# Kernel optimization log

Hardware: AMD Instinct MI355X
Metric: run time of the kernel (lower is better)

The kernel has to match this reference:

```python
import jax, jax.numpy as jnp
import numpy as np

N = 20000      # nodes
E = 320000     # directed edges (avg degree 16)
H = 4          # GAT attention heads
IN, HID, OUT = 5, 64, 32
DIMS = [(HID, HID), (HID, HID), (HID, OUT)]  # per-layer (in, out_per_head)


def setup_inputs() -> dict:
    keys = iter(jax.random.split(jax.random.key(0), 64))

    def rn(shape, s=0.1):
        return jax.random.normal(next(keys), shape, jnp.float32) * s

    inp = {
        "x": jax.random.normal(next(keys), (N, IN), jnp.float32),
        "edge_index": jax.random.randint(next(keys), (2, E), 0, N, dtype=jnp.int32),
        "enc_W": rn((IN, HID)), "enc_b": rn((HID,)),
    }
    for l, (din, dout) in enumerate(DIMS):
        inp["W%d" % l] = rn((din, H * dout))
        inp["as%d" % l] = rn((H, dout))
        inp["ad%d" % l] = rn((H, dout))
        inp["b%d" % l] = rn((dout,))
        inp["g%d" % l] = 1.0 + rn((dout,))
        inp["be%d" % l] = rn((dout,))
        inp["m%d" % l] = rn((dout,))
        inp["v%d" % l] = 1.0 + 0.1 * jax.random.uniform(next(keys), (dout,), jnp.float32)
    for h in ("eth", "man"):
        inp[h + "_W1"] = rn((OUT, OUT // 2)); inp[h + "_b1"] = rn((OUT // 2,))
        inp[h + "_W2"] = rn((OUT // 2, 1)); inp[h + "_b2"] = rn((1,))
    return inp


def _gat(x, src, dst, W, a_s, a_d, bias, n):
    # PyG GATConv: heads=H, concat=False (head mean), leaky_relu slope 0.2
    xp = (x @ W).reshape(n, H, -1)                        # [N,H,C]
    al_s = (xp * a_s).sum(-1)                             # [N,H]
    al_d = (xp * a_d).sum(-1)                             # [N,H]
    e = jax.nn.leaky_relu(al_s[src] + al_d[dst], 0.2)     # [E',H]
    emax = jax.ops.segment_max(e, dst, num_segments=n)    # stable softmax over in-edges
    ee = jnp.exp(e - emax[dst])
    den = jax.ops.segment_sum(ee, dst, num_segments=n)
    alpha = ee / (den[dst] + 1e-16)                       # [E',H]
    out = jax.ops.segment_sum(alpha[:, :, None] * xp[src], dst, num_segments=n)
    return out.mean(axis=1) + bias                        # [N,C]


def _bn(x, g, b, m, v):
    # BatchNorm1d, eval mode with running stats
    return (x - m) / jnp.sqrt(v + 1e-5) * g + b


def _head(z, W1, b1, W2, b2):
    # Linear -> ReLU -> (dropout off) -> Linear -> Sigmoid
    return jax.nn.sigmoid(jax.nn.relu(z @ W1 + b1) @ W2 + b2)


def _forward(x, src, dst, enc_W, enc_b, Ws, ASs, ADs, Bs, Gs, BEs, Ms, Vs, eth, man):
    n = x.shape[0]
    h = x @ enc_W + enc_b
    for l in range(3):
        h = _gat(h, src, dst, Ws[l], ASs[l], ADs[l], Bs[l], n)
        h = _bn(h, Gs[l], BEs[l], Ms[l], Vs[l])
        if l < 2:
            h = jax.nn.relu(h)
    graph_emb = h.mean(axis=0, keepdims=True)             # no `batch` attr branch
    ethics = _head(graph_emb, *eth)
    manip = _head(graph_emb, *man)
    return h, graph_emb, ethics, manip


def reference(x, edge_index, enc_W, enc_b,
              W0, as0, ad0, b0, g0, be0, m0, v0,
              W1, as1, ad1, b1, g1, be1, m1, v1,
              W2, as2, ad2, b2, g2, be2, m2, v2,
              eth_W1, eth_b1, eth_W2, eth_b2,
              man_W1, man_b1, man_W2, man_b2):
    n = x.shape[0]
    loops = jnp.arange(n, dtype=edge_index.dtype)
    src = jnp.concatenate([edge_index[0], loops])         # GATConv adds self-loops
    dst = jnp.concatenate([edge_index[1], loops])
    return _forward(x, src, dst, enc_W, enc_b,
                    [W0, W1, W2], [as0, as1, as2], [ad0, ad1, ad2], [b0, b1, b2],
                    [g0, g1, g2], [be0, be1, be2], [m0, m1, m2], [v0, v1, v2],
                    (eth_W1, eth_b1, eth_W2, eth_b2),
                    (man_W1, man_b1, man_W2, man_b2))
```

## Files before the change

### kernel.cpp

```cpp
#include <hip/hip_runtime.h>
#include <math.h>


#define H4 4

static __device__ __forceinline__ unsigned short f2bf(float f) {
  unsigned u = __float_as_uint(f);
  u += 0x7fffu + ((u >> 16) & 1u);
  return (unsigned short)(u >> 16);
}

static __device__ __forceinline__ float bfh(unsigned u) {
  return __uint_as_float(u << 16);
}
static __device__ __forceinline__ float bfl(unsigned u) {
  return __uint_as_float(u & 0xffff0000u);
}

__global__ void k_count(const int* __restrict__ dst, int* __restrict__ deg, int E) {
  int gid = blockIdx.x * blockDim.x + threadIdx.x;
  if (gid < E) atomicAdd(&deg[dst[gid]], 1);
}

__global__ void k_alloc(int* __restrict__ cursor, int* __restrict__ rbeg,
                        int* __restrict__ rend, int* __restrict__ col,
                        int* __restrict__ counter, int N,
                        const float* __restrict__ W0, const float* __restrict__ as0, const float* __restrict__ ad0,
                        const float* __restrict__ W1, const float* __restrict__ as1, const float* __restrict__ ad1,
                        const float* __restrict__ W2, const float* __restrict__ as2, const float* __restrict__ ad2,
                        float* __restrict__ pas, float* __restrict__ pad) {
  int gid = blockIdx.x * blockDim.x + threadIdx.x;
  int lane = threadIdx.x & 63;
  int size = (gid < N) ? (cursor[gid] + 1) : 0;
  int v = size;
#pragma unroll
  for (int off = 1; off < 64; off <<= 1) {
    int t = __shfl_up(v, off, 64);
    if (lane >= off) v += t;
  }
  int tot = __shfl(v, 63, 64);
  int base = 0;
  if (lane == 63) base = atomicAdd(counter, tot);
  base = __shfl(base, 63, 64);
  if (gid < N) {
    int p = base + v - size;
    rbeg[gid] = p;
    rend[gid] = p + size;
    col[p] = gid;
    cursor[gid] = p + 1;
  }
  if (blockIdx.x < 3) {
    int l = blockIdx.x;
    const float* W  = (l == 0) ? W0 : (l == 1) ? W1 : W2;
    const float* ap = (l == 0) ? as0 : (l == 1) ? as1 : as2;
    const float* dp = (l == 0) ? ad0 : (l == 1) ? ad1 : ad2;
    int HC = (l == 2) ? 128 : 256;
    int C  = HC / H4;
    int tid = threadIdx.x;
    int k = tid >> 2, h = tid & 3;
    float vs = 0.f, vd = 0.f;
    for (int c = 0; c < C; ++c) {
      float w = W[k * HC + h * C + c];
      vs += w * ap[h * C + c];
      vd += w * dp[h * C + c];
    }
    pas[l * 256 + tid] = vs;
    pad[l * 256 + tid] = vd;
  }
}

__global__ void k_scatter(const int* __restrict__ src, const int* __restrict__ dst,
                          int* __restrict__ cursor, int* __restrict__ col, int E) {
  int gid = blockIdx.x * blockDim.x + threadIdx.x;
  if (gid < E) {
    int p = atomicAdd(&cursor[dst[gid]], 1);
    col[p] = src[gid];
  }
}

template <int HC, bool ENC>
__global__ void k_gemm_al(const float* __restrict__ hin,
                          const float* __restrict__ encW, const float* __restrict__ encb,
                          const float* __restrict__ W,
                          const float* __restrict__ was, const float* __restrict__ wad,
                          unsigned short* __restrict__ xpb,
                          float* __restrict__ als, float* __restrict__ ald, int N) {
  constexpr int K = 64, NB = 16;
  __shared__ float hs[NB * K];
  int n0 = blockIdx.x * NB;
  int tid = threadIdx.x;
  if (ENC) {
    for (int idx = tid; idx < NB * K; idx += HC) {
      int i = idx >> 6, j = idx & 63;
      int n = n0 + i;
      float a = 0.f;
      if (n < N) {
        a = encb[j];
#pragma unroll
        for (int k = 0; k < 5; ++k) a += hin[n * 5 + k] * encW[k * 64 + j];
      }
      hs[idx] = a;
    }
  } else {
    for (int idx = tid; idx < NB * K; idx += HC) {
      int n = n0 + (idx >> 6);
      hs[idx] = (n < N) ? hin[(size_t)n0 * K + idx] : 0.f;
    }
  }
  __syncthreads();
  float acc[NB];
#pragma unroll
  for (int i = 0; i < NB; ++i) acc[i] = 0.f;
  for (int k = 0; k < K; k += 4) {
    float w0 = W[(k + 0) * HC + tid];
    float w1 = W[(k + 1) * HC + tid];
    float w2 = W[(k + 2) * HC + tid];
    float w3 = W[(k + 3) * HC + tid];
#pragma unroll
    for (int i = 0; i < NB; ++i) {
      float4 hv = *(const float4*)&hs[i * K + k];
      acc[i] += hv.x * w0 + hv.y * w1 + hv.z * w2 + hv.w * w3;
    }
  }
#pragma unroll
  for (int i = 0; i < NB; ++i) {
    int n = n0 + i;
    if (n < N) xpb[(size_t)n * HC + tid] = f2bf(acc[i]);
  }
  if (tid < NB * H4) {
    int i = tid >> 2, h = tid & 3;
    int n = n0 + i;
    float vs = 0.f, vd = 0.f;
#pragma unroll 8
    for (int k = 0; k < K; ++k) {
      float hv = hs[i * K + k];
      vs += hv * was[k * 4 + h];
      vd += hv * wad[k * 4 + h];
    }
    if (n < N) {
      als[n * H4 + h] = vs;
      ald[n * H4 + h] = vd;
    }
  }
}

template <int C, bool RELU, bool POOL>
__global__ __launch_bounds__(128) void k_gather(
    const unsigned short* __restrict__ xpb,
    const float* __restrict__ als, const float* __restrict__ ald,
    const int* __restrict__ rbeg, const int* __restrict__ rend,
    const int* __restrict__ col,
    const float* __restrict__ bias, const float* __restrict__ g,
    const float* __restrict__ be, const float* __restrict__ m,
    const float* __restrict__ v, float* __restrict__ hout,
    float* __restrict__ gpart, int N) {
  constexpr int HC = H4 * C;
  constexpr int VPL = HC / 64;
  __shared__ float accbuf[HC];
  __shared__ float sbuf[H4];
  int sub = threadIdx.x >> 6;
  int lane = threadIdx.x & 63;
  int n = blockIdx.x;
  int h = lane >> 4;
  float aldn = ald[n * H4 + h];
  int beg = rbeg[n], end = rend[n];
  int len = end - beg;
  int lenA = (len + 1) >> 1;
  int jb = sub ? (beg + lenA) : beg;
  int je = sub ? end : (beg + lenA);

  float s = 0.f;
  float acc[VPL];
#pragma unroll
  for (int i = 0; i < VPL; ++i) acc[i] = 0.f;

  int j = jb;
  for (; j + 3 < je; j += 4) {
    int s0 = col[j], s1 = col[j + 1], s2 = col[j + 2], s3 = col[j + 3];
    float a0 = als[s0 * H4 + h], a1 = als[s1 * H4 + h];
    float a2 = als[s2 * H4 + h], a3 = als[s3 * H4 + h];
    float e0 = a0 + aldn; e0 = (e0 > 0.f) ? e0 : 0.2f * e0; e0 = __expf(e0);
    float e1 = a1 + aldn; e1 = (e1 > 0.f) ? e1 : 0.2f * e1; e1 = __expf(e1);
    float e2 = a2 + aldn; e2 = (e2 > 0.f) ? e2 : 0.2f * e2; e2 = __expf(e2);
    float e3 = a3 + aldn; e3 = (e3 > 0.f) ? e3 : 0.2f * e3; e3 = __expf(e3);
    s += (e0 + e1) + (e2 + e3);
    if constexpr (VPL == 4) {
      uint2 u0 = *(const uint2*)(xpb + (size_t)s0 * HC + lane * 4);
      uint2 u1 = *(const uint2*)(xpb + (size_t)s1 * HC + lane * 4);
      uint2 u2 = *(const uint2*)(xpb + (size_t)s2 * HC + lane * 4);
      uint2 u3 = *(const uint2*)(xpb + (size_t)s3 * HC + lane * 4);
      acc[0] += e0 * bfh(u0.x) + e1 * bfh(u1.x) + e2 * bfh(u2.x) + e3 * bfh(u3.x);
      acc[1] += e0 * bfl(u0.x) + e1 * bfl(u1.x) + e2 * bfl(u2.x) + e3 * bfl(u3.x);
      acc[2] += e0 * bfh(u0.y) + e1 * bfh(u1.y) + e2 * bfh(u2.y) + e3 * bfh(u3.y);
      acc[3] += e0 * bfl(u0.y) + e1 * bfl(u1.y) + e2 * bfl(u2.y) + e3 * bfl(u3.y);
    } else {
      unsigned u0 = *(const unsigned*)(xpb + (size_t)s0 * HC + lane * 2);
      unsigned u1 = *(const unsigned*)(xpb + (size_t)s1 * HC + lane * 2);
      unsigned u2 = *(const unsigned*)(xpb + (size_t)s2 * HC + lane * 2);
      unsigned u3 = *(const unsigned*)(xpb + (size_t)s3 * HC + lane * 2);
      acc[0] += e0 * bfh(u0) + e1 * bfh(u1) + e2 * bfh(u2) + e3 * bfh(u3);
      acc[1] += e0 * bfl(u0) + e1 * bfl(u1) + e2 * bfl(u2) + e3 * bfl(u3);
    }
  }
  for (; j < je; ++j) {
    int s0 = col[j];
    float a0 = als[s0 * H4 + h];
    float e0 = a0 + aldn; e0 = (e0 > 0.f) ? e0 : 0.2f * e0; e0 = __expf(e0);
    s += e0;
    if constexpr (VPL == 4) {
      uint2 u0 = *(const uint2*)(xpb + (size_t)s0 * HC + lane * 4);
      acc[0] += e0 * bfh(u0.x);
      acc[1] += e0 * bfl(u0.x);
      acc[2] += e0 * bfh(u0.y);
      acc[3] += e0 * bfl(u0.y);
    } else {
      unsigned u0 = *(const unsigned*)(xpb + (size_t)s0 * HC + lane * 2);
      acc[0] += e0 * bfh(u0);
      acc[1] += e0 * bfl(u0);
    }
  }

  if (sub) {
    if ((lane & 15) == 0) sbuf[h] = s;
#pragma unroll
    for (int i = 0; i < VPL; ++i) accbuf[lane * VPL + i] = acc[i];
  }
  __syncthreads();
  if (sub) return;
  s += sbuf[h];
#pragma unroll
  for (int i = 0; i < VPL; ++i) acc[i] += accbuf[lane * VPL + i];

  float inv = 1.f / (s + 1e-16f);
#pragma unroll
  for (int i = 0; i < VPL; ++i) {
    acc[i] *= inv;
    acc[i] += __shfl_xor(acc[i], 16, 64);
    acc[i] += __shfl_xor(acc[i], 32, 64);
  }

  if (lane < 16) {
    int c0 = lane * VPL;
    float o[VPL];
#pragma unroll
    for (int i = 0; i < VPL; ++i) {
      int cc = c0 + i;
      float t = acc[i] * (1.f / H4) + bias[cc];
      t = (t - m[cc]) * rsqrtf(v[cc] + 1e-5f) * g[cc] + be[cc];
      if (RELU) t = fmaxf(t, 0.f);
      o[i] = t;
      if (POOL) atomicAdd(&gpart[(blockIdx.x & 255) * 32 + cc], t);
    }
    if constexpr (VPL == 4)
      *(float4*)&hout[(size_t)n * C + c0] = make_float4(o[0], o[1], o[2], o[3]);
    else
      *(float2*)&hout[(size_t)n * C + c0] = make_float2(o[0], o[1]);
  }
}

__global__ void k_heads2(const float* __restrict__ gpart,
                         const float* __restrict__ eW1, const float* __restrict__ eb1,
                         const float* __restrict__ eW2, const float* __restrict__ eb2,
                         const float* __restrict__ mW1, const float* __restrict__ mb1,
                         const float* __restrict__ mW2, const float* __restrict__ mb2,
                         float* __restrict__ out, int N) {
  __shared__ float red[256];
  __shared__ float z[32];
  __shared__ float hid[32];
  int tid = threadIdx.x;
  int c = tid & 31;
  float s = 0.f;
  for (int b = tid >> 5; b < 256; b += 8) s += gpart[b * 32 + c];
  red[tid] = s;
  __syncthreads();
  size_t base = (size_t)N * 32;
  if (tid < 32) {
    float t = 0.f;
#pragma unroll
    for (int i = 0; i < 8; ++i) t += red[i * 32 + tid];
    t /= (float)N;
    z[tid] = t;
    out[base + tid] = t;
  }
  __syncthreads();
  if (tid < 16) {
    float a = eb1[tid], b = mb1[tid];
    for (int k = 0; k < 32; ++k) {
      a += z[k] * eW1[k * 16 + tid];
      b += z[k] * mW1[k * 16 + tid];
    }
    hid[tid] = fmaxf(a, 0.f);
    hid[16 + tid] = fmaxf(b, 0.f);
  }
  __syncthreads();
  if (tid == 0) {
    float a = eb2[0];
    for (int k = 0; k < 16; ++k) a += hid[k] * eW2[k];
    out[base + 32] = 1.f / (1.f + __expf(-a));
  } else if (tid == 1) {
    float a = mb2[0];
    for (int k = 0; k < 16; ++k) a += hid[16 + k] * mW2[k];
    out[base + 33] = 1.f / (1.f + __expf(-a));
  }
}

extern "C" void kernel_launch(void* const* d_in, const int* in_sizes, int n_in,
                              void* d_out, int out_size, void* d_ws, size_t ws_size,
                              hipStream_t stream) {
  const int N = in_sizes[0] / 5;
  const int E = in_sizes[1] / 2;
  const int M = E + N;

  const float* x = (const float*)d_in[0];
  const int* ei = (const int*)d_in[1];
  const int* e_src = ei;
  const int* e_dst = ei + E;
  const float* encW = (const float*)d_in[2];
  const float* encb = (const float*)d_in[3];
  const float* Wl[3]; const float* asl[3]; const float* adl[3]; const float* bl[3];
  const float* gl[3]; const float* bel[3]; const float* ml[3]; const float* vl[3];
  for (int l = 0; l < 3; ++l) {
    const int o = 4 + 8 * l;
    Wl[l]  = (const float*)d_in[o + 0];
    asl[l] = (const float*)d_in[o + 1];
    adl[l] = (const float*)d_in[o + 2];
    bl[l]  = (const float*)d_in[o + 3];
    gl[l]  = (const float*)d_in[o + 4];
    bel[l] = (const float*)d_in[o + 5];
    ml[l]  = (const float*)d_in[o + 6];
    vl[l]  = (const float*)d_in[o + 7];
  }
  const float* eW1 = (const float*)d_in[28];
  const float* eb1 = (const float*)d_in[29];
  const float* eW2 = (const float*)d_in[30];
  const float* eb2 = (const float*)d_in[31];
  const float* mW1 = (const float*)d_in[32];
  const float* mb1 = (const float*)d_in[33];
  const float* mW2 = (const float*)d_in[34];
  const float* mb2 = (const float*)d_in[35];

  float* out = (float*)d_out;

  float* wf = (float*)d_ws;
  size_t off = 0;
  float* hA   = wf + off; off += (size_t)N * 64;
  float* hB   = wf + off; off += (size_t)N * 64;
  unsigned short* xpb = (unsigned short*)(wf + off); off += (size_t)N * 128;
  float* als  = wf + off; off += (size_t)N * 4;
  float* ald  = wf + off; off += (size_t)N * 4;
  float* pas  = wf + off; off += 3 * 256;
  float* pad  = wf + off; off += 3 * 256;
  int* wi = (int*)(wf + off);
  int* col     = wi;
  int* rbeg    = col + M;
  int* rend    = rbeg + N;
  int* cursor  = rend + N;
  int* counter = cursor + N;
  float* gpart = (float*)(counter + 1);

  const int T = 256;
  const int gE  = (E + T - 1) / T;
  const int gN  = (N + T - 1) / T;
  const int gGE = (N + 15) / 16;

  hipMemsetAsync(cursor, 0, (size_t)(N + 1) * sizeof(int) + 256 * 32 * sizeof(float), stream);
  k_count<<<gE, T, 0, stream>>>(e_dst, cursor, E);
  k_alloc<<<gN, T, 0, stream>>>(cursor, rbeg, rend, col, counter, N,
                                Wl[0], asl[0], adl[0], Wl[1], asl[1], adl[1],
                                Wl[2], asl[2], adl[2], pas, pad);
  k_scatter<<<gE, T, 0, stream>>>(e_src, e_dst, cursor, col, E);

  k_gemm_al<256, true><<<gGE, 256, 0, stream>>>(x, encW, encb, Wl[0], pas, pad,
                                                xpb, als, ald, N);
  k_gather<64, true, false><<<N, 128, 0, stream>>>(xpb, als, ald, rbeg, rend, col,
                                                   bl[0], gl[0], bel[0], ml[0], vl[0],
                                                   hB, gpart, N);

  k_gemm_al<256, false><<<gGE, 256, 0, stream>>>(hB, encW, encb, Wl[1], pas + 256, pad + 256,
                                                 xpb, als, ald, N);
  k_gather<64, true, false><<<N, 128, 0, stream>>>(xpb, als, ald, rbeg, rend, col,
                                                   bl[1], gl[1], bel[1], ml[1], vl[1],
                                                   hA, gpart, N);

  k_gemm_al<128, false><<<gGE, 128, 0, stream>>>(hA, encW, encb, Wl[2], pas + 512, pad + 512,
                                                 xpb, als, ald, N);
  k_gather<32, false, true><<<N, 128, 0, stream>>>(xpb, als, ald, rbeg, rend, col,
                                                   bl[2], gl[2], bel[2], ml[2], vl[2],
                                                   out, gpart, N);

  k_heads2<<<1, 256, 0, stream>>>(gpart, eW1, eb1, eW2, eb2, mW1, mb1, mW2, mb2, out, N);
}
```

Before: 332.9 us.

## Fuse whole GAT forward into one persistent cooperative kernel with grid syncs

Replaces the sequence of separate kernel launches (memset, CSR build, three gemm/gather pairs, heads) with a single cooperative persistent kernel that separates stages with grid.sync. The degree count runs concurrently with the first-layer GEMM on disjoint block subsets, and the gather switches from a two-wavefront-per-node block to one wavefront per node with a grid-stride loop. This removes launch overhead and inter-kernel gaps, but adds grid barrier costs and limits the grid to resident blocks, which may reduce latency hiding in the memory-bound gathers. A fallback multi-kernel path is kept in case the cooperative launch fails.

```diff
diff --git a/kernel.cpp b/kernel.cpp
--- a/kernel.cpp
+++ b/kernel.cpp
@@ -1,20 +1,316 @@
 #include <hip/hip_runtime.h>
+#include <hip/hip_cooperative_groups.h>
 #include <math.h>
 
 
+namespace cg = cooperative_groups;
+
 #define H4 4
+constexpr int TB = 256;
 
 static __device__ __forceinline__ unsigned short f2bf(float f) {
   unsigned u = __float_as_uint(f);
   u += 0x7fffu + ((u >> 16) & 1u);
   return (unsigned short)(u >> 16);
 }
-
-static __device__ __forceinline__ float bfh(unsigned u) {
-  return __uint_as_float(u << 16);
-}
-static __device__ __forceinline__ float bfl(unsigned u) {
-  return __uint_as_float(u & 0xffff0000u);
+static __device__ __forceinline__ float bfh(unsigned u) { return __uint_as_float(u << 16); }
+static __device__ __forceinline__ float bfl(unsigned u) { return __uint_as_float(u & 0xffff0000u); }
+
+struct Pr {
+  const float* x; const int* esrc; const int* edst;
+  const float* encW; const float* encb;
+  const float* W[3]; const float* as_[3]; const float* ad[3];
+  const float* b[3]; const float* g[3]; const float* be[3];
+  const float* m[3]; const float* v[3];
+  const float* eW1; const float* eb1; const float* eW2; const float* eb2;
+  const float* mW1; const float* mb1; const float* mW2; const float* mb2;
+  float* hA; float* hB; unsigned short* xpb; float* als; float* ald;
+  float* pas; float* pad; float* gpart;
+  int* col; int* rbeg; int* rend; int* cursor; int* counter;
+  float* out; int N; int E;
+};
+
+
+template <int HC, bool ENC>
+__device__ void gemm_stage(const Pr& p, const float* hin, const float* W,
+                           const float* was, const float* wad, float* hs,
+                           int bstart, int bnum) {
+  int b = (int)blockIdx.x - bstart;
+  if (b < 0 || b >= bnum) return;
+  int tid = threadIdx.x;
+  int ntile = (p.N + 15) >> 4;
+  for (int t = b; t < ntile; t += bnum) {
+    int n0 = t << 4;
+    for (int idx = tid; idx < 1024; idx += TB) {
+      int i = idx >> 6, j = idx & 63;
+      int n = n0 + i;
+      float a = 0.f;
+      if (ENC) {
+        if (n < p.N) {
+          a = p.encb[j];
+#pragma unroll
+          for (int k = 0; k < 5; ++k) a += p.x[n * 5 + k] * p.encW[k * 64 + j];
+        }
+      } else {
+        a = (n < p.N) ? hin[(size_t)n * 64 + j] : 0.f;
+      }
+      hs[idx] = a;
+    }
+    __syncthreads();
+    if (tid < HC) {
+      float acc[16];
+#pragma unroll
+      for (int i = 0; i < 16; ++i) acc[i] = 0.f;
+      for (int k = 0; k < 64; k += 4) {
+        float w0 = W[(k + 0) * HC + tid];
+        float w1 = W[(k + 1) * HC + tid];
+        float w2 = W[(k + 2) * HC + tid];
+        float w3 = W[(k + 3) * HC + tid];
+#pragma unroll
+        for (int i = 0; i < 16; ++i) {
+          float4 hv = *(const float4*)&hs[i * 64 + k];
+          acc[i] += hv.x * w0 + hv.y * w1 + hv.z * w2 + hv.w * w3;
+        }
+      }
+#pragma unroll
+      for (int i = 0; i < 16; ++i) {
+        int n = n0 + i;
+        if (n < p.N) p.xpb[(size_t)n * HC + tid] = f2bf(acc[i]);
+      }
+    }
+    if (tid < 64) {
+      int i = tid >> 2, h = tid & 3;
+      int n = n0 + i;
+      float vs = 0.f, vd = 0.f;
+#pragma unroll 8
+      for (int k = 0; k < 64; ++k) {
+        float hv = hs[i * 64 + k];
+        vs += hv * was[k * 4 + h];
+        vd += hv * wad[k * 4 + h];
+      }
+      if (n < p.N) {
+        p.als[n * H4 + h] = vs;
+        p.ald[n * H4 + h] = vd;
+      }
+    }
+    __syncthreads();
+  }
+}
+
+template <int C, bool RELU, bool POOL>
+__device__ void gather_stage(const Pr& p, float* hout, const float* bias,
+                             const float* g, const float* be, const float* m,
+                             const float* v) {
+  constexpr int HC = H4 * C;
+  constexpr int VPL = HC / 64;
+  int lane = threadIdx.x & 63;
+  int h = lane >> 4;
+  int wid = blockIdx.x * 4 + (threadIdx.x >> 6);
+  int wstride = gridDim.x * 4;
+  for (int n = wid; n < p.N; n += wstride) {
+    float aldn = p.ald[n * H4 + h];
+    int beg = p.rbeg[n], end = p.rend[n];
+    float s = 0.f;
+    float acc[VPL];
+#pragma unroll
+    for (int i = 0; i < VPL; ++i) acc[i] = 0.f;
+    int j = beg;
+    for (; j + 3 < end; j += 4) {
+      int s0 = p.col[j], s1 = p.col[j + 1], s2 = p.col[j + 2], s3 = p.col[j + 3];
+      float a0 = p.als[s0 * H4 + h], a1 = p.als[s1 * H4 + h];
+      float a2 = p.als[s2 * H4 + h], a3 = p.als[s3 * H4 + h];
+      float e0 = a0 + aldn; e0 = (e0 > 0.f) ? e0 : 0.2f * e0; e0 = __expf(e0);
+      float e1 = a1 + aldn; e1 = (e1 > 0.f) ? e1 : 0.2f * e1; e1 = __expf(e1);
+      float e2 = a2 + aldn; e2 = (e2 > 0.f) ? e2 : 0.2f * e2; e2 = __expf(e2);
+      float e3 = a3 + aldn; e3 = (e3 > 0.f) ? e3 : 0.2f * e3; e3 = __expf(e3);
+      s += (e0 + e1) + (e2 + e3);
+      if constexpr (VPL == 4) {
+        uint2 u0 = *(const uint2*)(p.xpb + (size_t)s0 * HC + lane * 4);
+        uint2 u1 = *(const uint2*)(p.xpb + (size_t)s1 * HC + lane * 4);
+        uint2 u2 = *(const uint2*)(p.xpb + (size_t)s2 * HC + lane * 4);
+        uint2 u3 = *(const uint2*)(p.xpb + (size_t)s3 * HC + lane * 4);
+        acc[0] += e0 * bfh(u0.x) + e1 * bfh(u1.x) + e2 * bfh(u2.x) + e3 * bfh(u3.x);
+        acc[1] += e0 * bfl(u0.x) + e1 * bfl(u1.x) + e2 * bfl(u2.x) + e3 * bfl(u3.x);
+        acc[2] += e0 * bfh(u0.y) + e1 * bfh(u1.y) + e2 * bfh(u2.y) + e3 * bfh(u3.y);
+        acc[3] += e0 * bfl(u0.y) + e1 * bfl(u1.y) + e2 * bfl(u2.y) + e3 * bfl(u3.y);
+      } else {
+        unsigned u0 = *(const unsigned*)(p.xpb + (size_t)s0 * HC + lane * 2);
+        unsigned u1 = *(const unsigned*)(p.xpb + (size_t)s1 * HC + lane * 2);
+        unsigned u2 = *(const unsigned*)(p.xpb + (size_t)s2 * HC + lane * 2);
+        unsigned u3 = *(const unsigned*)(p.xpb + (size_t)s3 * HC + lane * 2);
+        acc[0] += e0 * bfh(u0) + e1 * bfh(u1) + e2 * bfh(u2) + e3 * bfh(u3);
+        acc[1] += e0 * bfl(u0) + e1 * bfl(u1) + e2 * bfl(u2) + e3 * bfl(u3);
+      }
+    }
+    for (; j < end; ++j) {
+      int s0 = p.col[j];
+      float a0 = p.als[s0 * H4 + h];
+      float e0 = a0 + aldn; e0 = (e0 > 0.f) ? e0 : 0.2f * e0; e0 = __expf(e0);
+      s += e0;
+      if constexpr (VPL == 4) {
+        uint2 u0 = *(const uint2*)(p.xpb + (size_t)s0 * HC + lane * 4);
+        acc[0] += e0 * bfh(u0.x);
+        acc[1] += e0 * bfl(u0.x);
+        acc[2] += e0 * bfh(u0.y);
+        acc[3] += e0 * bfl(u0.y);
+      } else {
+        unsigned u0 = *(const unsigned*)(p.xpb + (size_t)s0 * HC + lane * 2);
+        acc[0] += e0 * bfh(u0);
+        acc[1] += e0 * bfl(u0);
+      }
+    }
+    float inv = 1.f / (s + 1e-16f);
+#pragma unroll
+    for (int i = 0; i < VPL; ++i) {
+      acc[i] *= inv;
+      acc[i] += __shfl_xor(acc[i], 16, 64);
+      acc[i] += __shfl_xor(acc[i], 32, 64);
+    }
+    if (lane < 16) {
+      int c0 = lane * VPL;
+      float o[VPL];
+#pragma unroll
+      for (int i = 0; i < VPL; ++i) {
+        int cc = c0 + i;
+        float t = acc[i] * (1.f / H4) + bias[cc];
+        t = (t - m[cc]) * rsqrtf(v[cc] + 1e-5f) * g[cc] + be[cc];
+        if (RELU) t = fmaxf(t, 0.f);
+        o[i] = t;
+        if (POOL) atomicAdd(&p.gpart[(n & 255) * 32 + cc], t);
+      }
+      if constexpr (VPL == 4)
+        *(float4*)&hout[(size_t)n * C + c0] = make_float4(o[0], o[1], o[2], o[3]);
+      else
+        *(float2*)&hout[(size_t)n * C + c0] = make_float2(o[0], o[1]);
+    }
+  }
+}
+
+__global__ __launch_bounds__(TB, 4) void mega(Pr p) {
+  cg::grid_group grid = cg::this_grid();
+  __shared__ float hs[1024];
+  const int tid = threadIdx.x;
+  const int lane = tid & 63;
+  const int GBx = gridDim.x;
+  const int gtid = blockIdx.x * TB + tid;
+  const int GS = GBx * TB;
+
+  {
+    int Z = p.N + 1 + 256 * 32;
+    int* zb = p.cursor;
+    for (int i = gtid; i < Z; i += GS) zb[i] = 0;
+    if (blockIdx.x < 3) {
+      int l = blockIdx.x;
+      const float* W = p.W[l];
+      const float* ap = p.as_[l];
+      const float* dp = p.ad[l];
+      int HC = (l == 2) ? 128 : 256;
+      int C = HC / H4;
+      int k = tid >> 2, h = tid & 3;
+      float vs = 0.f, vd = 0.f;
+      for (int c = 0; c < C; ++c) {
+        float w = W[k * HC + h * C + c];
+        vs += w * ap[h * C + c];
+        vd += w * dp[h * C + c];
+      }
+      p.pas[l * 256 + tid] = vs;
+      p.pad[l * 256 + tid] = vd;
+    }
+  }
+  grid.sync();
+
+  {
+    int cnt = GBx >> 2;
+    if ((int)blockIdx.x < cnt) {
+      for (int i = blockIdx.x * TB + tid; i < p.E; i += cnt * TB)
+        atomicAdd(&p.cursor[p.edst[i]], 1);
+    } else {
+      gemm_stage<256, true>(p, p.x, p.W[0], p.pas, p.pad, hs, cnt, GBx - cnt);
+    }
+  }
+  grid.sync();
+
+  for (int base = blockIdx.x * TB + (tid & ~63); base < p.N; base += GS) {
+    int gid = base + lane;
+    int dval = (gid < p.N) ? atomicAdd(&p.cursor[gid], 0) : -1;
+    int size = (gid < p.N) ? dval + 1 : 0;
+    int v = size;
+#pragma unroll
+    for (int off = 1; off < 64; off <<= 1) {
+      int t = __shfl_up(v, off, 64);
+      if (lane >= off) v += t;
+    }
+    int tot = __shfl(v, 63, 64);
+    int b0 = 0;
+    if (lane == 63) b0 = atomicAdd(p.counter, tot);
+    b0 = __shfl(b0, 63, 64);
+    if (gid < p.N) {
+      int pos = b0 + v - size;
+      p.rbeg[gid] = pos;
+      p.rend[gid] = pos + size;
+      p.col[pos] = gid;
+      p.cursor[gid] = pos + 1;
+    }
+  }
+  grid.sync();
+
+  for (int i = gtid; i < p.E; i += GS) {
+    int pos = atomicAdd(&p.cursor[p.edst[i]], 1);
+    p.col[pos] = p.esrc[i];
+  }
+  grid.sync();
+
+  gather_stage<64, true, false>(p, p.hB, p.b[0], p.g[0], p.be[0], p.m[0], p.v[0]);
+  grid.sync();
+  gemm_stage<256, false>(p, p.hB, p.W[1], p.pas + 256, p.pad + 256, hs, 0, GBx);
+  grid.sync();
+  gather_stage<64, true, false>(p, p.hA, p.b[1], p.g[1], p.be[1], p.m[1], p.v[1]);
+  grid.sync();
+  gemm_stage<128, false>(p, p.hA, p.W[2], p.pas + 512, p.pad + 512, hs, 0, GBx);
+  grid.sync();
+  gather_stage<32, false, true>(p, p.out, p.b[2], p.g[2], p.be[2], p.m[2], p.v[2]);
+  grid.sync();
+
+  if (blockIdx.x == 0) {
+    float* red = hs;
+    float* z = hs + 256;
+    float* hid = hs + 288;
+    int c = tid & 31;
+    float sAcc = 0.f;
+    for (int bkt = tid >> 5; bkt < 256; bkt += 8)
+      sAcc += atomicAdd(&p.gpart[bkt * 32 + c], 0.f);
+    red[tid] = sAcc;
+    __syncthreads();
+    size_t base = (size_t)p.N * 32;
+    if (tid < 32) {
+      float t = 0.f;
+#pragma unroll
+      for (int i = 0; i < 8; ++i) t += red[i * 32 + tid];
+      t /= (float)p.N;
+      z[tid] = t;
+      p.out[base + tid] = t;
+    }
+    __syncthreads();
+    if (tid < 16) {
+      float a = p.eb1[tid], b = p.mb1[tid];
+      for (int k = 0; k < 32; ++k) {
+        a += z[k] * p.eW1[k * 16 + tid];
+        b += z[k] * p.mW1[k * 16 + tid];
+      }
+      hid[tid] = fmaxf(a, 0.f);
+      hid[16 + tid] = fmaxf(b, 0.f);
+    }
+    __syncthreads();
+    if (tid == 0) {
+      float a = p.eb2[0];
+      for (int k = 0; k < 16; ++k) a += hid[k] * p.eW2[k];
+      p.out[base + 32] = 1.f / (1.f + __expf(-a));
+    } else if (tid == 1) {
+      float a = p.mb2[0];
+      for (int k = 0; k < 16; ++k) a += hid[16 + k] * p.mW2[k];
+      p.out[base + 33] = 1.f / (1.f + __expf(-a));
+    }
+  }
 }
 
 __global__ void k_count(const int* __restrict__ dst, int* __restrict__ deg, int E) {
@@ -22,16 +318,10 @@
   if (gid < E) atomicAdd(&deg[dst[gid]], 1);
 }
 
-__global__ void k_alloc(int* __restrict__ cursor, int* __restrict__ rbeg,
-                        int* __restrict__ rend, int* __restrict__ col,
-                        int* __restrict__ counter, int N,
-                        const float* __restrict__ W0, const float* __restrict__ as0, const float* __restrict__ ad0,
-                        const float* __restrict__ W1, const float* __restrict__ as1, const float* __restrict__ ad1,
-                        const float* __restrict__ W2, const float* __restrict__ as2, const float* __restrict__ ad2,
-                        float* __restrict__ pas, float* __restrict__ pad) {
+__global__ void k_alloc(Pr p) {
   int gid = blockIdx.x * blockDim.x + threadIdx.x;
   int lane = threadIdx.x & 63;
-  int size = (gid < N) ? (cursor[gid] + 1) : 0;
+  int size = (gid < p.N) ? (p.cursor[gid] + 1) : 0;
   int v = size;
 #pragma unroll
   for (int off = 1; off < 64; off <<= 1) {
@@ -39,23 +329,23 @@
     if (lane >= off) v += t;
   }
   int tot = __shfl(v, 63, 64);
-  int base = 0;
-  if (lane == 63) base = atomicAdd(counter, tot);
-  base = __shfl(base, 63, 64);
-  if (gid < N) {
-    int p = base + v - size;
-    rbeg[gid] = p;
-    rend[gid] = p + size;
-    col[p] = gid;
-    cursor[gid] = p + 1;
+  int b0 = 0;
+  if (lane == 63) b0 = atomicAdd(p.counter, tot);
+  b0 = __shfl(b0, 63, 64);
+  if (gid < p.N) {
+    int pos = b0 + v - size;
+    p.rbeg[gid] = pos;
+    p.rend[gid] = pos + size;
+    p.col[pos] = gid;
+    p.cursor[gid] = pos + 1;
   }
   if (blockIdx.x < 3) {
     int l = blockIdx.x;
-    const float* W  = (l == 0) ? W0 : (l == 1) ? W1 : W2;
-    const float* ap = (l == 0) ? as0 : (l == 1) ? as1 : as2;
-    const float* dp = (l == 0) ? ad0 : (l == 1) ? ad1 : ad2;
+    const float* W = p.W[l];
+    const float* ap = p.as_[l];
+    const float* dp = p.ad[l];
     int HC = (l == 2) ? 128 : 256;
-    int C  = HC / H4;
+    int C = HC / H4;
     int tid = threadIdx.x;
     int k = tid >> 2, h = tid & 3;
     float vs = 0.f, vd = 0.f;
@@ -64,8 +354,8 @@
       vs += w * ap[h * C + c];
       vd += w * dp[h * C + c];
     }
-    pas[l * 256 + tid] = vs;
-    pad[l * 256 + tid] = vd;
+    p.pas[l * 256 + tid] = vs;
+    p.pad[l * 256 + tid] = vd;
   }
 }
 
@@ -79,228 +369,60 @@
 }
 
 template <int HC, bool ENC>
-__global__ void k_gemm_al(const float* __restrict__ hin,
-                          const float* __restrict__ encW, const float* __restrict__ encb,
-                          const float* __restrict__ W,
-                          const float* __restrict__ was, const float* __restrict__ wad,
-                          unsigned short* __restrict__ xpb,
-                          float* __restrict__ als, float* __restrict__ ald, int N) {
-  constexpr int K = 64, NB = 16;
-  __shared__ float hs[NB * K];
-  int n0 = blockIdx.x * NB;
-  int tid = threadIdx.x;
-  if (ENC) {
-    for (int idx = tid; idx < NB * K; idx += HC) {
-      int i = idx >> 6, j = idx & 63;
-      int n = n0 + i;
-      float a = 0.f;
-      if (n < N) {
-        a = encb[j];
-#pragma unroll
-        for (int k = 0; k < 5; ++k) a += hin[n * 5 + k] * encW[k * 64 + j];
-      }
-      hs[idx] = a;
-    }
-  } else {
-    for (int idx = tid; idx < NB * K; idx += HC) {
-      int n = n0 + (idx >> 6);
-      hs[idx] = (n < N) ? hin[(size_t)n0 * K + idx] : 0.f;
-    }
-  }
-  __syncthreads();
-  float acc[NB];
-#pragma unroll
-  for (int i = 0; i < NB; ++i) acc[i] = 0.f;
-  for (int k = 0; k < K; k += 4) {
-    float w0 = W[(k + 0) * HC + tid];
-    float w1 = W[(k + 1) * HC + tid];
-    float w2 = W[(k + 2) * HC + tid];
-    float w3 = W[(k + 3) * HC + tid];
-#pragma unroll
-    for (int i = 0; i < NB; ++i) {
-      float4 hv = *(const float4*)&hs[i * K + k];
-      acc[i] += hv.x * w0 + hv.y * w1 + hv.z * w2 + hv.w * w3;
-    }
-  }
-#pragma unroll
-  for (int i = 0; i < NB; ++i) {
-    int n = n0 + i;
-    if (n < N) xpb[(size_t)n * HC + tid] = f2bf(acc[i]);
-  }
-  if (tid < NB * H4) {
-    int i = tid >> 2, h = tid & 3;
-    int n = n0 + i;
-    float vs = 0.f, vd = 0.f;
-#pragma unroll 8
-    for (int k = 0; k < K; ++k) {
-      float hv = hs[i * K + k];
-      vs += hv * was[k * 4 + h];
-      vd += hv * wad[k * 4 + h];
-    }
-    if (n < N) {
-      als[n * H4 + h] = vs;
-      ald[n * H4 + h] = vd;
-    }
-  }
+__global__ void k_gemm_al(Pr p, const float* __restrict__ hin, const float* __restrict__ W,
+                          const float* __restrict__ was, const float* __restrict__ wad) {
+  __shared__ float hs[1024];
+  gemm_stage<HC, ENC>(p, hin, W, was, wad, hs, 0, gridDim.x);
 }
 
 template <int C, bool RELU, bool POOL>
-__global__ __launch_bounds__(128) void k_gather(
-    const unsigned short* __restrict__ xpb,
-    const float* __restrict__ als, const float* __restrict__ ald,
-    const int* __restrict__ rbeg, const int* __restrict__ rend,
-    const int* __restrict__ col,
-    const float* __restrict__ bias, const float* __restrict__ g,
-    const float* __restrict__ be, const float* __restrict__ m,
-    const float* __restrict__ v, float* __restrict__ hout,
-    float* __restrict__ gpart, int N) {
-  constexpr int HC = H4 * C;
-  constexpr int VPL = HC / 64;
-  __shared__ float accbuf[HC];
-  __shared__ float sbuf[H4];
-  int sub = threadIdx.x >> 6;
-  int lane = threadIdx.x & 63;
-  int n = blockIdx.x;
-  int h = lane >> 4;
-  float aldn = ald[n * H4 + h];
-  int beg = rbeg[n], end = rend[n];
-  int len = end - beg;
-  int lenA = (len + 1) >> 1;
-  int jb = sub ? (beg + lenA) : beg;
-  int je = sub ? end : (beg + lenA);
-
-  float s = 0.f;
-  float acc[VPL];
-#pragma unroll
-  for (int i = 0; i < VPL; ++i) acc[i] = 0.f;
-
-  int j = jb;
-  for (; j + 3 < je; j += 4) {
-    int s0 = col[j], s1 = col[j + 1], s2 = col[j + 2], s3 = col[j + 3];
-    float a0 = als[s0 * H4 + h], a1 = als[s1 * H4 + h];
-    float a2 = als[s2 * H4 + h], a3 = als[s3 * H4 + h];
-    float e0 = a0 + aldn; e0 = (e0 > 0.f) ? e0 : 0.2f * e0; e0 = __expf(e0);
-    float e1 = a1 + aldn; e1 = (e1 > 0.f) ? e1 : 0.2f * e1; e1 = __expf(e1);
-    float e2 = a2 + aldn; e2 = (e2 > 0.f) ? e2 : 0.2f * e2; e2 = __expf(e2);
-    float e3 = a3 + aldn; e3 = (e3 > 0.f) ? e3 : 0.2f * e3; e3 = __expf(e3);
-    s += (e0 + e1) + (e2 + e3);
-    if constexpr (VPL == 4) {
-      uint2 u0 = *(const uint2*)(xpb + (size_t)s0 * HC + lane * 4);
-      uint2 u1 = *(const uint2*)(xpb + (size_t)s1 * HC + lane * 4);
-      uint2 u2 = *(const uint2*)(xpb + (size_t)s2 * HC + lane * 4);
-      uint2 u3 = *(const uint2*)(xpb + (size_t)s3 * HC + lane * 4);
-      acc[0] += e0 * bfh(u0.x) + e1 * bfh(u1.x) + e2 * bfh(u2.x) + e3 * bfh(u3.x);
-      acc[1] += e0 * bfl(u0.x) + e1 * bfl(u1.x) + e2 * bfl(u2.x) + e3 * bfl(u3.x);
-      acc[2] += e0 * bfh(u0.y) + e1 * bfh(u1.y) + e2 * bfh(u2.y) + e3 * bfh(u3.y);
-      acc[3] += e0 * bfl(u0.y) + e1 * bfl(u1.y) + e2 * bfl(u2.y) + e3 * bfl(u3.y);
-    } else {
-      unsigned u0 = *(const unsigned*)(xpb + (size_t)s0 * HC + lane * 2);
-      unsigned u1 = *(const unsigned*)(xpb + (size_t)s1 * HC + lane * 2);
-      unsigned u2 = *(const unsigned*)(xpb + (size_t)s2 * HC + lane * 2);
-      unsigned u3 = *(const unsigned*)(xpb + (size_t)s3 * HC + lane * 2);
-      acc[0] += e0 * bfh(u0) + e1 * bfh(u1) + e2 * bfh(u2) + e3 * bfh(u3);
-      acc[1] += e0 * bfl(u0) + e1 * bfl(u1) + e2 * bfl(u2) + e3 * bfl(u3);
-    }
-  }
-  for (; j < je; ++j) {
-    int s0 = col[j];
-    float a0 = als[s0 * H4 + h];
-    float e0 = a0 + aldn; e0 = (e0 > 0.f) ? e0 : 0.2f * e0; e0 = __expf(e0);
-    s += e0;
-    if constexpr (VPL == 4) {
-      uint2 u0 = *(const uint2*)(xpb + (size_t)s0 * HC + lane * 4);
-      acc[0] += e0 * bfh(u0.x);
-      acc[1] += e0 * bfl(u0.x);
-      acc[2] += e0 * bfh(u0.y);
-      acc[3] += e0 * bfl(u0.y);
-    } else {
-      unsigned u0 = *(const unsigned*)(xpb + (size_t)s0 * HC + lane * 2);
-      acc[0] += e0 * bfh(u0);
-      acc[1] += e0 * bfl(u0);
-    }
-  }
-
-  if (sub) {
-    if ((lane & 15) == 0) sbuf[h] = s;
-#pragma unroll
-    for (int i = 0; i < VPL; ++i) accbuf[lane * VPL + i] = acc[i];
-  }
-  __syncthreads();
-  if (sub) return;
-  s += sbuf[h];
-#pragma unroll
-  for (int i = 0; i < VPL; ++i) acc[i] += accbuf[lane * VPL + i];
-
-  float inv = 1.f / (s + 1e-16f);
-#pragma unroll
-  for (int i = 0; i < VPL; ++i) {
-    acc[i] *= inv;
-    acc[i] += __shfl_xor(acc[i], 16, 64);
-    acc[i] += __shfl_xor(acc[i], 32, 64);
-  }
-
-  if (lane < 16) {
-    int c0 = lane * VPL;
-    float o[VPL];
-#pragma unroll
-    for (int i = 0; i < VPL; ++i) {
-      int cc = c0 + i;
-      float t = acc[i] * (1.f / H4) + bias[cc];
-      t = (t - m[cc]) * rsqrtf(v[cc] + 1e-5f) * g[cc] + be[cc];
-      if (RELU) t = fmaxf(t, 0.f);
-      o[i] = t;
-      if (POOL) atomicAdd(&gpart[(blockIdx.x & 255) * 32 + cc], t);
-    }
-    if constexpr (VPL == 4)
-      *(float4*)&hout[(size_t)n * C + c0] = make_float4(o[0], o[1], o[2], o[3]);
-    else
-      *(float2*)&hout[(size_t)n * C + c0] = make_float2(o[0], o[1]);
-  }
-}
-
-__global__ void k_heads2(const float* __restrict__ gpart,
-                         const float* __restrict__ eW1, const float* __restrict__ eb1,
-                         const float* __restrict__ eW2, const float* __restrict__ eb2,
-                         const float* __restrict__ mW1, const float* __restrict__ mb1,
-                         const float* __restrict__ mW2, const float* __restrict__ mb2,
-                         float* __restrict__ out, int N) {
+__global__ __launch_bounds__(256) void k_gather(Pr p, float* hout,
+                                                const float* __restrict__ bias,
+                                                const float* __restrict__ g,
+                                                const float* __restrict__ be,
+                                                const float* __restrict__ m,
+                                                const float* __restrict__ v) {
+  gather_stage<C, RELU, POOL>(p, hout, bias, g, be, m, v);
+}
+
+__global__ void k_heads2(Pr p) {
   __shared__ float red[256];
   __shared__ float z[32];
   __shared__ float hid[32];
   int tid = threadIdx.x;
   int c = tid & 31;
   float s = 0.f;
-  for (int b = tid >> 5; b < 256; b += 8) s += gpart[b * 32 + c];
+  for (int b = tid >> 5; b < 256; b += 8) s += p.gpart[b * 32 + c];
   red[tid] = s;
   __syncthreads();
-  size_t base = (size_t)N * 32;
+  size_t base = (size_t)p.N * 32;
   if (tid < 32) {
     float t = 0.f;
 #pragma unroll
     for (int i = 0; i < 8; ++i) t += red[i * 32 + tid];
-    t /= (float)N;
+    t /= (float)p.N;
     z[tid] = t;
-    out[base + tid] = t;
+    p.out[base + tid] = t;
   }
   __syncthreads();
   if (tid < 16) {
-    float a = eb1[tid], b = mb1[tid];
+    float a = p.eb1[tid], b = p.mb1[tid];
     for (int k = 0; k < 32; ++k) {
-      a += z[k] * eW1[k * 16 + tid];
-      b += z[k] * mW1[k * 16 + tid];
+      a += z[k] * p.eW1[k * 16 + tid];
+      b += z[k] * p.mW1[k * 16 + tid];
     }
     hid[tid] = fmaxf(a, 0.f);
     hid[16 + tid] = fmaxf(b, 0.f);
   }
   __syncthreads();
   if (tid == 0) {
-    float a = eb2[0];
-    for (int k = 0; k < 16; ++k) a += hid[k] * eW2[k];
-    out[base + 32] = 1.f / (1.f + __expf(-a));
+    float a = p.eb2[0];
+    for (int k = 0; k < 16; ++k) a += hid[k] * p.eW2[k];
+    p.out[base + 32] = 1.f / (1.f + __expf(-a));
   } else if (tid == 1) {
-    float a = mb2[0];
-    for (int k = 0; k < 16; ++k) a += hid[16 + k] * mW2[k];
-    out[base + 33] = 1.f / (1.f + __expf(-a));
+    float a = p.mb2[0];
+    for (int k = 0; k < 16; ++k) a += hid[16 + k] * p.mW2[k];
+    p.out[base + 33] = 1.f / (1.f + __expf(-a));
   }
 }
 
@@ -311,82 +433,78 @@
   const int E = in_sizes[1] / 2;
   const int M = E + N;
 
-  const float* x = (const float*)d_in[0];
+  Pr p;
+  p.x = (const float*)d_in[0];
   const int* ei = (const int*)d_in[1];
-  const int* e_src = ei;
-  const int* e_dst = ei + E;
-  const float* encW = (const float*)d_in[2];
-  const float* encb = (const float*)d_in[3];
-  const float* Wl[3]; const float* asl[3]; const float* adl[3]; const float* bl[3];
-  const float* gl[3]; const float* bel[3]; const float* ml[3]; const float* vl[3];
+  p.esrc = ei;
+  p.edst = ei + E;
+  p.encW = (const float*)d_in[2];
+  p.encb = (const float*)d_in[3];
   for (int l = 0; l < 3; ++l) {
     const int o = 4 + 8 * l;
-    Wl[l]  = (const float*)d_in[o + 0];
-    asl[l] = (const float*)d_in[o + 1];
-    adl[l] = (const float*)d_in[o + 2];
-    bl[l]  = (const float*)d_in[o + 3];
-    gl[l]  = (const float*)d_in[o + 4];
-    bel[l] = (const float*)d_in[o + 5];
-    ml[l]  = (const float*)d_in[o + 6];
-    vl[l]  = (const float*)d_in[o + 7];
-  }
-  const float* eW1 = (const float*)d_in[28];
-  const float* eb1 = (const float*)d_in[29];
-  const float* eW2 = (const float*)d_in[30];
-  const float* eb2 = (const float*)d_in[31];
-  const float* mW1 = (const float*)d_in[32];
-  const float* mb1 = (const float*)d_in[33];
-  const float* mW2 = (const float*)d_in[34];
-  const float* mb2 = (const float*)d_in[35];
-
-  float* out = (float*)d_out;
+    p.W[l]  = (const float*)d_in[o + 0];
+    p.as_[l] = (const float*)d_in[o + 1];
+    p.ad[l] = (const float*)d_in[o + 2];
+    p.b[l]  = (const float*)d_in[o + 3];
+    p.g[l]  = (const float*)d_in[o + 4];
+    p.be[l] = (const float*)d_in[o + 5];
+    p.m[l]  = (const float*)d_in[o + 6];
+    p.v[l]  = (const float*)d_in[o + 7];
+  }
+  p.eW1 = (const float*)d_in[28]; p.eb1 = (const float*)d_in[29];
+  p.eW2 = (const float*)d_in[30]; p.eb2 = (const float*)d_in[31];
+  p.mW1 = (const float*)d_in[32]; p.mb1 = (const float*)d_in[33];
+  p.mW2 = (const float*)d_in[34]; p.mb2 = (const float*)d_in[35];
+  p.out = (float*)d_out;
+  p.N = N; p.E = E;
 
   float* wf = (float*)d_ws;
   size_t off = 0;
-  float* hA   = wf + off; off += (size_t)N * 64;
-  float* hB   = wf + off; off += (size_t)N * 64;
-  unsigned short* xpb = (unsigned short*)(wf + off); off += (size_t)N * 128;
-  float* als  = wf + off; off += (size_t)N * 4;
-  float* ald  = wf + off; off += (size_t)N * 4;
-  float* pas  = wf + off; off += 3 * 256;
-  float* pad  = wf + off; off += 3 * 256;
+  p.hA = wf + off; off += (size_t)N * 64;
+  p.hB = wf + off; off += (size_t)N * 64;
+  p.xpb = (unsigned short*)(wf + off); off += (size_t)N * 128;
+  p.als = wf + off; off += (size_t)N * 4;
+  p.ald = wf + off; off += (size_t)N * 4;
+  p.pas = wf + off; off += 3 * 256;
+  p.pad = wf + off; off += 3 * 256;
   int* wi = (int*)(wf + off);
-  int* col     = wi;
-  int* rbeg    = col + M;
-  int* rend    = rbeg + N;
-  int* cursor  = rend + N;
-  int* counter = cursor + N;
-  float* gpart = (float*)(counter + 1);
+  p.col = wi;
+  p.rbeg = wi + M;
+  p.rend = p.rbeg + N;
+  p.cursor = p.rend + N;
+  p.counter = p.cursor + N;
+  p.gpart = (float*)(p.counter + 1);
+
+  hipError_t st = hipErrorUnknown;
+  int maxB = 0;
+  if (hipOccupancyMaxActiveBlocksPerMultiprocessor(&maxB, (const void*)mega, TB, 0)
+      != hipSuccess) maxB = 0;
+  if (maxB > 4) maxB = 4;
+  int gb = maxB * 256;
+  if (gb >= 256) {
+    void* args[] = {&p};
+    st = hipLaunchCooperativeKernel((const void*)mega, dim3(gb), dim3(TB), args, 0, stream);
+  }
+  if (st == hipSuccess) return;
 
   const int T = 256;
-  const int gE  = (E + T - 1) / T;
-  const int gN  = (N + T - 1) / T;
+  const int gE = (E + T - 1) / T;
+  const int gN = (N + T - 1) / T;
   const int gGE = (N + 15) / 16;
 
-  hipMemsetAsync(cursor, 0, (size_t)(N + 1) * sizeof(int) + 256 * 32 * sizeof(float), stream);
-  k_count<<<gE, T, 0, stream>>>(e_dst, cursor, E);
-  k_alloc<<<gN, T, 0, stream>>>(cursor, rbeg, rend, col, counter, N,
-                                Wl[0], asl[0], adl[0], Wl[1], asl[1], adl[1],
-                                Wl[2], asl[2], adl[2], pas, pad);
-  k_scatter<<<gE, T, 0, stream>>>(e_src, e_dst, cursor, col, E);
-
-  k_gemm_al<256, true><<<gGE, 256, 0, stream>>>(x, encW, encb, Wl[0], pas, pad,
-                                                xpb, als, ald, N);
-  k_gather<64, true, false><<<N, 128, 0, stream>>>(xpb, als, ald, rbeg, rend, col,
-                                                   bl[0], gl[0], bel[0], ml[0], vl[0],
-                                                   hB, gpart, N);
-
-  k_gemm_al<256, false><<<gGE, 256, 0, stream>>>(hB, encW, encb, Wl[1], pas + 256, pad + 256,
-                                                 xpb, als, ald, N);
-  k_gather<64, true, false><<<N, 128, 0, stream>>>(xpb, als, ald, rbeg, rend, col,
-                                                   bl[1], gl[1], bel[1], ml[1], vl[1],
-                                                   hA, gpart, N);
-
-  k_gemm_al<128, false><<<gGE, 128, 0, stream>>>(hA, encW, encb, Wl[2], pas + 512, pad + 512,
-                                                 xpb, als, ald, N);
-  k_gather<32, false, true><<<N, 128, 0, stream>>>(xpb, als, ald, rbeg, rend, col,
-                                                   bl[2], gl[2], bel[2], ml[2], vl[2],
-                                                   out, gpart, N);
-
-  k_heads2<<<1, 256, 0, stream>>>(gpart, eW1, eb1, eW2, eb2, mW1, mb1, mW2, mb2, out, N);
-}
+  hipMemsetAsync(p.cursor, 0, (size_t)(N + 1) * sizeof(int) + 256 * 32 * sizeof(float), stream);
+  k_count<<<gE, T, 0, stream>>>(p.edst, p.cursor, E);
+  k_alloc<<<gN, T, 0, stream>>>(p);
+  k_scatter<<<gE, T, 0, stream>>>(p.esrc, p.edst, p.cursor, p.col, E);
+
+  k_gemm_al<256, true><<<gGE, 256, 0, stream>>>(p, p.x, p.W[0], p.pas, p.pad);
+  k_gather<64, true, false><<<(N + 3) / 4, 256, 0, stream>>>(p, p.hB, p.b[0], p.g[0],
+                                                             p.be[0], p.m[0], p.v[0]);
+  k_gemm_al<256, false><<<gGE, 256, 0, stream>>>(p, p.hB, p.W[1], p.pas + 256, p.pad + 256);
+  k_gather<64, true, false><<<(N + 3) / 4, 256, 0, stream>>>(p, p.hA, p.b[1], p.g[1],
+                                                             p.be[1], p.m[1], p.v[1]);
+  k_gemm_al<128, false><<<gGE, 128, 0, stream>>>(p, p.hA, p.W[2], p.pas + 512, p.pad + 512);
+  k_gather<32, false, true><<<(N + 3) / 4, 256, 0, stream>>>(p, p.out, p.b[2], p.g[2],
+                                                             p.be[2], p.m[2], p.v[2]);
+  k_heads2<<<1, 256, 0, stream>>>(p);
+}
```

After: 947.1 us. +184.5%, slower.
